# Kernel optimization log

Hardware: AMD Instinct MI355X
Metric: run time of the kernel (lower is better)

The kernel has to match this reference:

```python
import jax, jax.numpy as jnp
import numpy as np

K = 1024
H = 16
HID = 4 * K
EPS = 1e-5


def _layernorm(x, g, b):
    mu = jnp.mean(x, axis=-1, keepdims=True)
    var = jnp.var(x, axis=-1, keepdims=True)
    return (x - mu) * jax.lax.rsqrt(var + EPS) * g + b


def _attention(xq, xkv, wq, wk, wv, wo, bo, causal):
    b, t, e = xq.shape
    tc = xkv.shape[1]
    h, s = H, e // H
    scale = e ** (-0.25)  # applied to both q and k, as in the original
    q = (xq @ wq).reshape(b, t, h, s) * scale
    k = (xkv @ wk).reshape(b, tc, h, s) * scale
    v = (xkv @ wv).reshape(b, tc, h, s)
    dot = jnp.einsum('bqhs,bkhs->bhqk', q, k)  # (b,h,t,tc)
    if causal:
        mask = jnp.tril(jnp.ones((t, tc), dtype=bool))
        dot = jnp.where(mask, dot, jnp.finfo(dot.dtype).min)
    att = jax.nn.softmax(dot, axis=-1)
    out = jnp.einsum('bhqk,bkhs->bqhs', att, v).reshape(b, t, e)
    return out @ wo + bo


def setup_inputs() -> dict:
    key = jax.random.key(0)
    ks = jax.random.split(key, 16)
    sd = K ** -0.5
    inp = {
        'x': jax.random.normal(ks[0], (4, 1024, K), jnp.float32),
        'context': jax.random.normal(ks[1], (4, 1024, K), jnp.float32),
        'sa_wq': jax.random.normal(ks[2], (K, K), jnp.float32) * sd,
        'sa_wk': jax.random.normal(ks[3], (K, K), jnp.float32) * sd,
        'sa_wv': jax.random.normal(ks[4], (K, K), jnp.float32) * sd,
        'sa_wo': jax.random.normal(ks[5], (K, K), jnp.float32) * sd,
        'sa_bo': jnp.zeros((K,), jnp.float32),
        'ca_wq': jax.random.normal(ks[6], (K, K), jnp.float32) * sd,
        'ca_wk': jax.random.normal(ks[7], (K, K), jnp.float32) * sd,
        'ca_wv': jax.random.normal(ks[8], (K, K), jnp.float32) * sd,
        'ca_wo': jax.random.normal(ks[9], (K, K), jnp.float32) * sd,
        'ca_bo': jnp.zeros((K,), jnp.float32),
        'n1_g': jnp.ones((K,), jnp.float32), 'n1_b': jnp.zeros((K,), jnp.float32),
        'n2_g': jnp.ones((K,), jnp.float32), 'n2_b': jnp.zeros((K,), jnp.float32),
        'n3_g': jnp.ones((K,), jnp.float32), 'n3_b': jnp.zeros((K,), jnp.float32),
        'ff_w1': jax.random.normal(ks[10], (K, HID), jnp.float32) * sd,
        'ff_b1': jnp.zeros((HID,), jnp.float32),
        'ff_w2': jax.random.normal(ks[11], (HID, K), jnp.float32) * (HID ** -0.5),
        'ff_b2': jnp.zeros((K,), jnp.float32),
    }
    return inp


def reference(x, context, sa_wq, sa_wk, sa_wv, sa_wo, sa_bo,
              ca_wq, ca_wk, ca_wv, ca_wo, ca_bo,
              n1_g, n1_b, n2_g, n2_b, n3_g, n3_b,
              ff_w1, ff_b1, ff_w2, ff_b2):
    # Masked self-attention + residual + LN (dropout is identity in eval mode)
    sa = _attention(x, x, sa_wq, sa_wk, sa_wv, sa_wo, sa_bo, causal=True)
    x = _layernorm(x + sa, n1_g, n1_b)
    # Cross-attention + residual + LN
    ca = _attention(x, context, ca_wq, ca_wk, ca_wv, ca_wo, ca_bo, causal=False)
    x = _layernorm(x + ca, n2_g, n2_b)
    # FFN + residual + LN
    ff = jax.nn.relu(x @ ff_w1 + ff_b1) @ ff_w2 + ff_b2
    x = _layernorm(x + ff, n3_g, n3_b)
    return x
```

## Files before the change

### kernel.cpp

```cpp
#include <hip/hip_runtime.h>

typedef __bf16 bf16x8 __attribute__((ext_vector_type(8)));
typedef __bf16 bf16x4 __attribute__((ext_vector_type(4)));
typedef float floatx4 __attribute__((ext_vector_type(4)));

#define EMB 1024
#define MROWS 4096
#define HIDN 4096
#define PSTRIDE ((size_t)MROWS * EMB)

__device__ __forceinline__ void load_lds16(const __bf16* g, __bf16* l) {
    __builtin_amdgcn_global_load_lds(
        (const __attribute__((address_space(1))) void*)g,
        (__attribute__((address_space(3))) void*)l, 16, 0, 0);
}

struct TJobs { const float* s[16]; __bf16* d[16]; int sld[16]; int dld[16]; };
__global__ void transpose_cast16_kernel(TJobs a) {
    __shared__ float tile[32][33];
    int jz = blockIdx.z;
    const float* in = a.s[jz];
    __bf16* out = a.d[jz];
    int sld = a.sld[jz], dld = a.dld[jz];
    int tx = threadIdx.x, ty = threadIdx.y;
    int c0 = blockIdx.x * 32, r0 = blockIdx.y * 32;
#pragma unroll
    for (int i = 0; i < 32; i += 8)
        tile[ty + i][tx] = in[(size_t)(r0 + ty + i) * sld + c0 + tx];
    __syncthreads();
#pragma unroll
    for (int i = 0; i < 32; i += 8)
        out[(size_t)(c0 + ty + i) * dld + r0 + tx] = (__bf16)tile[tx][ty + i];
}

__global__ void transpose_v_kernel(const __bf16* __restrict__ in,
                                   __bf16* __restrict__ vt, int ld, int Tc) {
    __shared__ __bf16 tile[32][33];
    int tx = threadIdx.x, ty = threadIdx.y;
    int t0 = blockIdx.x * 32, s0 = blockIdx.y * 32;
    int bh = blockIdx.z, b = bh >> 4, h = bh & 15;
#pragma unroll
    for (int i = 0; i < 32; i += 8)
        tile[ty + i][tx] = in[(size_t)(b * Tc + t0 + ty + i) * ld + h * 64 + s0 + tx];
    __syncthreads();
#pragma unroll
    for (int i = 0; i < 32; i += 8)
        vt[((size_t)bh * 64 + s0 + ty + i) * Tc + t0 + tx] = tile[tx][ty + i];
}

__global__ void cast_bf16_kernel(const float* __restrict__ in,
                                 __bf16* __restrict__ out, int n) {
    int i = (blockIdx.x * 256 + threadIdx.x) * 4;
    if (i >= n) return;
    float4 v = *(const float4*)(in + i);
    bf16x4 o;
    o[0] = (__bf16)v.x; o[1] = (__bf16)v.y; o[2] = (__bf16)v.z; o[3] = (__bf16)v.w;
    *(bf16x4*)(out + i) = o;
}

template <int RELU, int REG>
__launch_bounds__(256, 4)
__global__ void gemm_bt(const __bf16* __restrict__ A, const __bf16* __restrict__ A2,
                        int asplit, const __bf16* __restrict__ Bt,
                        __bf16* __restrict__ cb, __bf16* __restrict__ cbalt,
                        const float* __restrict__ bias,
                        int M, int N, int Kd, float scale0, float scale1,
                        int split, int fx, int fy) {
    __shared__ alignas(16) __bf16 smem[2 * 128 * 32];
    __bf16* As = smem;
    __bf16* Bs = smem + 128 * 32;
    int tid  = threadIdx.x;
    int wv   = tid >> 6, lane = tid & 63;

    int L   = blockIdx.x + gridDim.x * (blockIdx.y + gridDim.y * blockIdx.z);
    int xcd = L & 7, j = L >> 3;
    int ff  = fx * fy;
    int zw  = xcd / ff;
    int rr  = xcd % ff;
    int nxf = gridDim.x / fx;
    int bnw = (j % nxf) * fx + (rr % fx);
    int bmw = (j / nxf) * fy + (rr / fx);
    int bn  = bnw * 128, bm = bmw * 128;

    int wm   = (wv & 1) * 64, wn = (wv >> 1) * 64;
    int l16  = lane & 15, g16 = lane >> 4;

    int kc   = Kd / gridDim.z;
    int zoff = zw * kc;

    const __bf16* Ause = (bn >= asplit) ? A2 : A;

    const __bf16* ag0 = Ause + (size_t)(bm + (tid >> 2)) * Kd + zoff + (tid & 3) * 8;
    const __bf16* ag1 = ag0 + (size_t)64 * Kd;
    const __bf16* bg0 = Bt + (size_t)(bn + (tid >> 2)) * Kd + zoff + (tid & 3) * 8;
    const __bf16* bg1 = bg0 + (size_t)64 * Kd;
    __bf16* al0 = &As[tid * 8];
    __bf16* al1 = &As[2048 + tid * 8];
    __bf16* bl0 = &Bs[tid * 8];
    __bf16* bl1 = &Bs[2048 + tid * 8];

    floatx4 acc[4][4] = {};

    if (REG) {
        bf16x8 pa0 = *(const bf16x8*)ag0;
        bf16x8 pa1 = *(const bf16x8*)ag1;
        bf16x8 pb0 = *(const bf16x8*)bg0;
        bf16x8 pb1 = *(const bf16x8*)bg1;
        for (int k0 = 0; k0 < kc; k0 += 32) {
            *(bf16x8*)al0 = pa0;
            *(bf16x8*)al1 = pa1;
            *(bf16x8*)bl0 = pb0;
            *(bf16x8*)bl1 = pb1;
            if (k0 + 32 < kc) {
                ag0 += 32; ag1 += 32; bg0 += 32; bg1 += 32;
                pa0 = *(const bf16x8*)ag0;
                pa1 = *(const bf16x8*)ag1;
                pb0 = *(const bf16x8*)bg0;
                pb1 = *(const bf16x8*)bg1;
            }
            __syncthreads();
            bf16x8 af[4], bfr[4];
#pragma unroll
            for (int i = 0; i < 4; ++i)
                af[i] = *(const bf16x8*)&As[(wm + i * 16 + l16) * 32 + g16 * 8];
#pragma unroll
            for (int jj = 0; jj < 4; ++jj)
                bfr[jj] = *(const bf16x8*)&Bs[(wn + jj * 16 + l16) * 32 + g16 * 8];
#pragma unroll
            for (int i = 0; i < 4; ++i)
#pragma unroll
                for (int jj = 0; jj < 4; ++jj)
                    acc[i][jj] = __builtin_amdgcn_mfma_f32_16x16x32_bf16(af[i], bfr[jj], acc[i][jj], 0, 0, 0);
            __syncthreads();
        }
    } else {
        for (int k0 = 0; k0 < kc; k0 += 32) {
            __syncthreads();
            load_lds16(ag0, al0); load_lds16(ag1, al1);
            load_lds16(bg0, bl0); load_lds16(bg1, bl1);
            ag0 += 32; ag1 += 32; bg0 += 32; bg1 += 32;
            __syncthreads();
            bf16x8 af[4], bfr[4];
#pragma unroll
            for (int i = 0; i < 4; ++i)
                af[i] = *(const bf16x8*)&As[(wm + i * 16 + l16) * 32 + g16 * 8];
#pragma unroll
            for (int jj = 0; jj < 4; ++jj)
                bfr[jj] = *(const bf16x8*)&Bs[(wn + jj * 16 + l16) * 32 + g16 * 8];
#pragma unroll
            for (int i = 0; i < 4; ++i)
#pragma unroll
                for (int jj = 0; jj < 4; ++jj)
                    acc[i][jj] = __builtin_amdgcn_mfma_f32_16x16x32_bf16(af[i], bfr[jj], acc[i][jj], 0, 0, 0);
        }
        __syncthreads();
    }

    __bf16* Cp = (zw == 0) ? cb : cbalt + (size_t)(zw - 1) * M * N;
    const float* bz = (zw == 0) ? bias : nullptr;

    __bf16* eb = smem + wv * 2048;
    int erow = lane >> 2;
    int ecol = (lane & 3) * 16;
#pragma unroll
    for (int i = 0; i < 4; ++i) {
#pragma unroll
        for (int jj = 0; jj < 4; ++jj) {
            int col  = bn + wn + jj * 16 + l16;
            float sc = (col < split) ? scale0 : scale1;
            float bv = bz ? bz[col] : 0.f;
#pragma unroll
            for (int r = 0; r < 4; ++r) {
                float v = acc[i][jj][r] * sc + bv;
                if (RELU) v = fmaxf(v, 0.f);
                eb[(g16 * 4 + r) * 76 + jj * 16 + l16] = (__bf16)v;
            }
        }
        bf16x8 t0 = *(const bf16x8*)&eb[erow * 76 + ecol];
        bf16x8 t1 = *(const bf16x8*)&eb[erow * 76 + ecol + 8];
        size_t gb = (size_t)(bm + wm + i * 16 + erow) * N + bn + wn + ecol;
        *(bf16x8*)&Cp[gb]     = t0;
        *(bf16x8*)&Cp[gb + 8] = t1;
    }
}


#define VM4 asm volatile("s_waitcnt vmcnt(4)" ::: "memory")
#define VM0 asm volatile("s_waitcnt vmcnt(0)" ::: "memory")

#define STG(GB, HROWS, LDST, TILE)                                             \
    do {                                                                       \
        load_lds16((GB) + (size_t)(HROWS) * Kd + (TILE) * 64, (LDST) + tid8);  \
        load_lds16((GB) + (size_t)((HROWS) + 128) * Kd + (TILE) * 64,          \
                   (LDST) + 4096 + tid8);                                      \
    } while (0)

#define PHASE(ABUF, BBUF, QM, QN, STAGE, TAIL)                                  \
    {                                                                           \
        bf16x8 a_[4][2], b_[2][2];                                              \
        _Pragma("unroll")                                                       \
        for (int i2 = 0; i2 < 4; ++i2) {                                        \
            int s_ = (QM) * 128 + wr64 + i2 * 16 + l16;                         \
            a_[i2][0] = *(const bf16x8*)&(ABUF)[s_ * 64 + pa0];                 \
            a_[i2][1] = *(const bf16x8*)&(ABUF)[s_ * 64 + pa1];                 \
        }                                                                       \
        _Pragma("unroll")                                                       \
        for (int j2 = 0; j2 < 2; ++j2) {                                        \
            int s_ = (QN) * 128 + wc32 + j2 * 16 + l16;                         \
            b_[j2][0] = *(const bf16x8*)&(BBUF)[s_ * 64 + pa0];                 \
            b_[j2][1] = *(const bf16x8*)&(BBUF)[s_ * 64 + pa1];                 \
        }                                                                       \
        STAGE;                                                                  \
        __builtin_amdgcn_s_barrier();                                           \
        asm volatile("s_waitcnt lgkmcnt(0)" ::: "memory");                      \
        __builtin_amdgcn_s_setprio(1);                                          \
        _Pragma("unroll")                                                       \
        for (int i2 = 0; i2 < 4; ++i2)                                          \
            _Pragma("unroll")                                                   \
            for (int j2 = 0; j2 < 2; ++j2) {                                    \
                acc[(QM) * 4 + i2][(QN) * 2 + j2] =                             \
                    __builtin_amdgcn_mfma_f32_16x16x32_bf16(                    \
                        a_[i2][0], b_[j2][0],                                   \
                        acc[(QM) * 4 + i2][(QN) * 2 + j2], 0, 0, 0);            \
                acc[(QM) * 4 + i2][(QN) * 2 + j2] =                             \
                    __builtin_amdgcn_mfma_f32_16x16x32_bf16(                    \
                        a_[i2][1], b_[j2][1],                                   \
                        acc[(QM) * 4 + i2][(QN) * 2 + j2], 0, 0, 0);            \
            }                                                                   \
        __builtin_amdgcn_s_setprio(0);                                          \
        TAIL;                                                                   \
        __builtin_amdgcn_s_barrier();                                           \
    }

template <int RELU>
__launch_bounds__(512, 2)
__global__ void gemm256(const __bf16* __restrict__ A, const __bf16* __restrict__ A2,
                        int asplit, const __bf16* __restrict__ Bt,
                        __bf16* __restrict__ C, const float* __restrict__ bias,
                        int N, int Kd, float scale0, float scale1,
                        int split, int pw) {
    __shared__ alignas(16) __bf16 smem[65536];
    __bf16* Alds0 = smem;
    __bf16* Alds1 = smem + 16384;
    __bf16* Blds0 = smem + 32768;
    __bf16* Blds1 = smem + 49152;

    int tid = threadIdx.x;
    int wv = tid >> 6, lane = tid & 63;
    int l16 = lane & 15, g16 = lane >> 4;
    int wr = wv >> 2, wc = wv & 3;
    int wr64 = wr * 64, wc32 = wc * 32;
    int pa0 = (g16 ^ (l16 & 7)) * 8;
    int pa1 = pa0 ^ 32;

    int L = blockIdx.x;
    int xcd = L & 7, jj = L >> 3;
    int bm = ((xcd >> 1) * 4 + jj / pw) * 256;
    int bn = ((xcd & 1) * pw + jj % pw) * 256;

    const __bf16* Ause = (bn >= asplit) ? A2 : A;
    int tid8 = tid * 8;
    int colOff = ((tid & 7) ^ ((tid >> 3) & 7)) * 8;
    const __bf16* baseA = Ause + (size_t)(bm + (tid >> 3)) * Kd + colOff;
    const __bf16* baseB = Bt + (size_t)(bn + (tid >> 8) * 64 + ((tid >> 3) & 31)) * Kd + colOff;

    floatx4 acc[8][4] = {};

    STG(baseA, 0,  Alds0,        0);
    STG(baseB, 0,  Blds0,        0);
    STG(baseA, 64, Alds0 + 8192, 0);
    STG(baseB, 32, Blds0 + 8192, 0);
    STG(baseA, 0,  Alds1,        1);
    STG(baseB, 0,  Blds1,        1);
    VM4;
    __builtin_amdgcn_s_barrier();

    int niter = Kd >> 7;
    for (int t = 0; t < niter - 1; ++t) {
        int tv = 2 * t + 1, tn0 = 2 * t + 2, tn1 = 2 * t + 3;
        PHASE(Alds0, Blds0, 0, 0, STG(baseA, 64, Alds1 + 8192, tv),  (void)0);
        PHASE(Alds0, Blds0, 0, 1, STG(baseB, 32, Blds1 + 8192, tv),  (void)0);
        PHASE(Alds0, Blds0, 1, 0, STG(baseA, 0,  Alds0,        tn0), (void)0);
        PHASE(Alds0, Blds0, 1, 1, STG(baseB, 0,  Blds0,        tn0), VM4);
        PHASE(Alds1, Blds1, 0, 0, STG(baseA, 64, Alds0 + 8192, tn0), (void)0);
        PHASE(Alds1, Blds1, 0, 1, STG(baseB, 32, Blds0 + 8192, tn0), (void)0);
        PHASE(Alds1, Blds1, 1, 0, STG(baseA, 0,  Alds1,        tn1), (void)0);
        PHASE(Alds1, Blds1, 1, 1, STG(baseB, 0,  Blds1,        tn1), VM4);
    }
    {
        int tv = (Kd >> 6) - 1;
        PHASE(Alds0, Blds0, 0, 0, STG(baseA, 64, Alds1 + 8192, tv), (void)0);
        PHASE(Alds0, Blds0, 0, 1, STG(baseB, 32, Blds1 + 8192, tv), (void)0);
        PHASE(Alds0, Blds0, 1, 0, (void)0, (void)0);
        PHASE(Alds0, Blds0, 1, 1, (void)0, VM0);
        PHASE(Alds1, Blds1, 0, 0, (void)0, (void)0);
        PHASE(Alds1, Blds1, 0, 1, (void)0, (void)0);
        PHASE(Alds1, Blds1, 1, 0, (void)0, (void)0);
        PHASE(Alds1, Blds1, 1, 1, (void)0, (void)0);
    }

    __syncthreads();

    __bf16* eb = smem + wv * 1216;
    int erow = lane >> 2;
    int ecol = (lane & 3) * 16;
    float sc[4], bv[4];
#pragma unroll
    for (int j = 0; j < 4; ++j) {
        int col = bn + wc * 64 + j * 16 + l16;
        sc[j] = (col < split) ? scale0 : scale1;
        bv[j] = bias ? bias[col] : 0.f;
    }
#pragma unroll
    for (int i = 0; i < 8; ++i) {
#pragma unroll
        for (int j = 0; j < 4; ++j) {
#pragma unroll
            for (int r = 0; r < 4; ++r) {
                float v = acc[i][j][r] * sc[j] + bv[j];
                if (RELU) v = fmaxf(v, 0.f);
                eb[(g16 * 4 + r) * 76 + j * 16 + l16] = (__bf16)v;
            }
        }
        bf16x8 t0 = *(const bf16x8*)&eb[erow * 76 + ecol];
        bf16x8 t1 = *(const bf16x8*)&eb[erow * 76 + ecol + 8];
        size_t gb = (size_t)(bm + wr * 128 + i * 16 + erow) * N + bn + wc * 64 + ecol;
        *(bf16x8*)&C[gb]     = t0;
        *(bf16x8*)&C[gb + 8] = t1;
    }
}

__launch_bounds__(256, 3)
__global__ void attn_kernel(const __bf16* __restrict__ qb, const __bf16* __restrict__ kb,
                            const __bf16* __restrict__ vt, int ldq, int ldk,
                            __bf16* __restrict__ out, int causal, int Tc) {
    constexpr int T = 1024;
    __shared__ alignas(16) __bf16 Qs[128 * 72];
    __shared__ alignas(16) __bf16 Ks[64 * 72];
    __shared__ alignas(16) __bf16 Vs[64 * 72];
    __shared__ alignas(16) __bf16 Ps[4][16 * 72];

    int tid = threadIdx.x;
    int wv = tid >> 6, lane = tid & 63;
    int l16 = lane & 15, g16 = lane >> 4;

    int L = blockIdx.x;
    int xcd = L & 7, idx = L >> 3;
    int i3 = idx & 7;
    int qt2 = (idx & 32) ? (7 - i3) : i3;
    int pair = xcd + 8 * (idx >> 3);
    int h = pair & 15, b = pair >> 4;

    int r0 = tid >> 3, s8 = (tid & 7) * 8;
    int r1 = r0 + 32;

#pragma unroll
    for (int p = 0; p < 4; ++p) {
        int row = r0 + p * 32;
        bf16x8 qv = *(const bf16x8*)(qb + (size_t)(b * T + qt2 * 128 + row) * ldq + h * 64 + s8);
        *(bf16x8*)&Qs[row * 72 + s8] = qv;
    }

    floatx4 oacc[2][4] = {};
    float li[2] = {0.f, 0.f};

    int ktend = causal ? (2 * qt2 + 2) : (Tc / 64);

    const __bf16* kbase = kb + (size_t)b * Tc * ldk + h * 64 + s8;
    const __bf16* vbase = vt + (size_t)(b * 16 + h) * 64 * Tc + s8;

    bf16x8 kc0 = *(const bf16x8*)(kbase + (size_t)r0 * ldk);
    bf16x8 kc1 = *(const bf16x8*)(kbase + (size_t)r1 * ldk);
    bf16x8 vc0 = *(const bf16x8*)(vbase + (size_t)r0 * Tc);
    bf16x8 vc1 = *(const bf16x8*)(vbase + (size_t)r1 * Tc);
    bf16x8 kn0, kn1, vn0, vn1;

    for (int kt = 0; kt < ktend; ++kt) {
        __syncthreads();
        *(bf16x8*)&Ks[r0 * 72 + s8] = kc0;
        *(bf16x8*)&Ks[r1 * 72 + s8] = kc1;
        *(bf16x8*)&Vs[r0 * 72 + s8] = vc0;
        *(bf16x8*)&Vs[r1 * 72 + s8] = vc1;
        if (kt + 1 < ktend) {
            const __bf16* kp = kbase + (size_t)(kt + 1) * 64 * ldk;
            const __bf16* vp = vbase + (size_t)(kt + 1) * 64;
            kn0 = *(const bf16x8*)(kp + (size_t)r0 * ldk);
            kn1 = *(const bf16x8*)(kp + (size_t)r1 * ldk);
            vn0 = *(const bf16x8*)(vp + (size_t)r0 * Tc);
            vn1 = *(const bf16x8*)(vp + (size_t)r1 * Tc);
        }
        __syncthreads();

#pragma unroll
        for (int sub = 0; sub < 2; ++sub) {
            if (causal && kt > 2 * qt2 + sub) continue;

            floatx4 sacc[4] = {};
#pragma unroll
            for (int kk = 0; kk < 2; ++kk) {
                bf16x8 bq = *(const bf16x8*)&Qs[(sub * 64 + wv * 16 + l16) * 72 + kk * 32 + g16 * 8];
#pragma unroll
                for (int j = 0; j < 4; ++j) {
                    bf16x8 ak = *(const bf16x8*)&Ks[(j * 16 + l16) * 72 + kk * 32 + g16 * 8];
                    sacc[j] = __builtin_amdgcn_mfma_f32_16x16x32_bf16(ak, bq, sacc[j], 0, 0, 0);
                }
            }
            if (causal && kt == 2 * qt2 + sub) {
                int qloc = wv * 16 + l16;
#pragma unroll
                for (int j = 0; j < 4; ++j)
#pragma unroll
                    for (int r = 0; r < 4; ++r)
                        if (j * 16 + g16 * 4 + r > qloc) sacc[j][r] = -1e30f;
            }

#pragma unroll
            for (int j = 0; j < 4; ++j) {
                bf16x4 pk;
#pragma unroll
                for (int r = 0; r < 4; ++r) {
                    float p = __builtin_amdgcn_exp2f(sacc[j][r]);
                    li[sub] += p;
                    pk[r] = (__bf16)p;
                }
                *(bf16x4*)&Ps[wv][l16 * 72 + j * 16 + g16 * 4] = pk;
            }
#pragma unroll
            for (int kk = 0; kk < 2; ++kk) {
                bf16x8 bp = *(const bf16x8*)&Ps[wv][l16 * 72 + kk * 32 + g16 * 8];
#pragma unroll
                for (int j = 0; j < 4; ++j) {
                    bf16x8 av = *(const bf16x8*)&Vs[(j * 16 + l16) * 72 + kk * 32 + g16 * 8];
                    oacc[sub][j] = __builtin_amdgcn_mfma_f32_16x16x32_bf16(av, bp, oacc[sub][j], 0, 0, 0);
                }
            }
        }
        kc0 = kn0; kc1 = kn1; vc0 = vn0; vc1 = vn1;
    }

    li[0] += __shfl_xor(li[0], 16); li[0] += __shfl_xor(li[0], 32);
    li[1] += __shfl_xor(li[1], 16); li[1] += __shfl_xor(li[1], 32);

    __syncthreads();
    int rw = lane >> 2, c4 = (lane & 3) * 16;
#pragma unroll
    for (int sub = 0; sub < 2; ++sub) {
        float inv = 1.f / li[sub];
#pragma unroll
        for (int j = 0; j < 4; ++j) {
            bf16x4 ok;
#pragma unroll
            for (int r = 0; r < 4; ++r) ok[r] = (__bf16)(oacc[sub][j][r] * inv);
            *(bf16x4*)&Ks[(wv * 16 + l16) * 72 + j * 16 + g16 * 4] = ok;
        }
        bf16x8 o0 = *(const bf16x8*)&Ks[(wv * 16 + rw) * 72 + c4];
        bf16x8 o1 = *(const bf16x8*)&Ks[(wv * 16 + rw) * 72 + c4 + 8];
        size_t ob = (size_t)(b * T + qt2 * 128 + sub * 64 + wv * 16 + rw) * EMB + h * 64 + c4;
        *(bf16x8*)&out[ob]     = o0;
        *(bf16x8*)&out[ob + 8] = o1;
    }
}

__launch_bounds__(256)
__global__ void ln_kernel(const float* __restrict__ res,
                          const __bf16* __restrict__ pb, int np,
                          const float* __restrict__ g, const float* __restrict__ be,
                          float* __restrict__ outf, __bf16* __restrict__ outb) {
    __shared__ float red[8];
    int row = blockIdx.x, tid = threadIdx.x;
    size_t base = (size_t)row * EMB;
    float4 v = ((const float4*)(res + base))[tid];
    for (int i = 0; i < np; ++i) {
        bf16x4 u = *(const bf16x4*)(pb + i * PSTRIDE + base + tid * 4);
        v.x += (float)u[0]; v.y += (float)u[1];
        v.z += (float)u[2]; v.w += (float)u[3];
    }
    float s  = v.x + v.y + v.z + v.w;
    float ss = v.x * v.x + v.y * v.y + v.z * v.z + v.w * v.w;
#pragma unroll
    for (int o = 1; o < 64; o <<= 1) { s += __shfl_xor(s, o); ss += __shfl_xor(ss, o); }
    if ((tid & 63) == 0) { red[(tid >> 6) * 2] = s; red[(tid >> 6) * 2 + 1] = ss; }
    __syncthreads();
    s  = red[0] + red[2] + red[4] + red[6];
    ss = red[1] + red[3] + red[5] + red[7];
    float mu  = s * (1.0f / 1024.0f);
    float var = ss * (1.0f / 1024.0f) - mu * mu;
    float rs  = rsqrtf(var + 1e-5f);
    float4 gg = ((const float4*)g)[tid];
    float4 bb = ((const float4*)be)[tid];
    float4 y;
    y.x = (v.x - mu) * rs * gg.x + bb.x;
    y.y = (v.y - mu) * rs * gg.y + bb.y;
    y.z = (v.z - mu) * rs * gg.z + bb.z;
    y.w = (v.w - mu) * rs * gg.w + bb.w;
    ((float4*)(outf + base))[tid] = y;
    if (outb) {
        bf16x4 o;
        o[0] = (__bf16)y.x; o[1] = (__bf16)y.y; o[2] = (__bf16)y.z; o[3] = (__bf16)y.w;
        *(bf16x4*)(outb + base + tid * 4) = o;
    }
}

extern "C" void kernel_launch(void* const* d_in, const int* in_sizes, int n_in,
                              void* d_out, int out_size, void* d_ws, size_t ws_size,
                              hipStream_t stream) {
    const float* x     = (const float*)d_in[0];
    const float* ctx   = (const float*)d_in[1];
    const float* sa_wq = (const float*)d_in[2];
    const float* sa_wk = (const float*)d_in[3];
    const float* sa_wv = (const float*)d_in[4];
    const float* sa_wo = (const float*)d_in[5];
    const float* sa_bo = (const float*)d_in[6];
    const float* ca_wq = (const float*)d_in[7];
    const float* ca_wk = (const float*)d_in[8];
    const float* ca_wv = (const float*)d_in[9];
    const float* ca_wo = (const float*)d_in[10];
    const float* ca_bo = (const float*)d_in[11];
    const float* n1_g = (const float*)d_in[12];
    const float* n1_b = (const float*)d_in[13];
    const float* n2_g = (const float*)d_in[14];
    const float* n2_b = (const float*)d_in[15];
    const float* n3_g = (const float*)d_in[16];
    const float* n3_b = (const float*)d_in[17];
    const float* ff_w1 = (const float*)d_in[18];
    const float* ff_b1 = (const float*)d_in[19];
    const float* ff_w2 = (const float*)d_in[20];
    const float* ff_b2 = (const float*)d_in[21];

    size_t off = 0;
    auto alloc = [&](size_t bytes) {
        void* p = (char*)d_ws + off;
        off += (bytes + 255) & ~(size_t)255;
        return p;
    };
    __bf16* w_sa_qkvT = (__bf16*)alloc((size_t)3 * EMB * EMB * 2);
    __bf16* w_sa_oT   = (__bf16*)alloc((size_t)EMB * EMB * 2);
    __bf16* w_ca_kvqT = (__bf16*)alloc((size_t)3 * EMB * EMB * 2);
    __bf16* w_ca_oT   = (__bf16*)alloc((size_t)EMB * EMB * 2);
    __bf16* w1T       = (__bf16*)alloc((size_t)HIDN * EMB * 2);
    __bf16* w2T       = (__bf16*)alloc((size_t)EMB * HIDN * 2);
    __bf16* xb        = (__bf16*)alloc((size_t)MROWS * EMB * 2);
    __bf16* qkv       = (__bf16*)alloc((size_t)MROWS * 3 * EMB * 2);
    __bf16* ao        = (__bf16*)alloc((size_t)MROWS * EMB * 2);
    __bf16* hid       = (__bf16*)alloc((size_t)MROWS * HIDN * 2);
    __bf16* x1b       = (__bf16*)alloc((size_t)MROWS * EMB * 2);
    __bf16* vt        = (__bf16*)alloc((size_t)MROWS * EMB * 2);
    float* res1       = (float*)alloc((size_t)MROWS * EMB * 4);
    float* res2       = (float*)alloc((size_t)MROWS * EMB * 4);

    __bf16* qkvc = qkv;
    __bf16* pbo  = qkv;
    __bf16* pbf  = xb;

    const float QSC = 0.04508422002778011f;
    const int   BIG = 1 << 30;
    dim3 tb(32, 8);

    TJobs tj;
    tj.s[0] = sa_wq; tj.d[0] = w_sa_qkvT;                          tj.sld[0] = EMB;  tj.dld[0] = EMB;
    tj.s[1] = sa_wk; tj.d[1] = w_sa_qkvT + (size_t)EMB * EMB;      tj.sld[1] = EMB;  tj.dld[1] = EMB;
    tj.s[2] = sa_wv; tj.d[2] = w_sa_qkvT + (size_t)2 * EMB * EMB;  tj.sld[2] = EMB;  tj.dld[2] = EMB;
    tj.s[3] = sa_wo; tj.d[3] = w_sa_oT;                            tj.sld[3] = EMB;  tj.dld[3] = EMB;
    tj.s[4] = ca_wk; tj.d[4] = w_ca_kvqT;                          tj.sld[4] = EMB;  tj.dld[4] = EMB;
    tj.s[5] = ca_wv; tj.d[5] = w_ca_kvqT + (size_t)EMB * EMB;      tj.sld[5] = EMB;  tj.dld[5] = EMB;
    tj.s[6] = ca_wq; tj.d[6] = w_ca_kvqT + (size_t)2 * EMB * EMB;  tj.sld[6] = EMB;  tj.dld[6] = EMB;
    tj.s[7] = ca_wo; tj.d[7] = w_ca_oT;                            tj.sld[7] = EMB;  tj.dld[7] = EMB;
    for (int c = 0; c < 4; ++c) {
        tj.s[8 + c] = ff_w1 + (size_t)c * 1024;
        tj.d[8 + c] = w1T + (size_t)c * 1024 * 1024;
        tj.sld[8 + c] = HIDN; tj.dld[8 + c] = EMB;
    }
    for (int c = 0; c < 4; ++c) {
        tj.s[12 + c] = ff_w2 + (size_t)c * 1024 * 1024;
        tj.d[12 + c] = w2T + (size_t)c * 1024;
        tj.sld[12 + c] = EMB; tj.dld[12 + c] = HIDN;
    }
    transpose_cast16_kernel<<<dim3(32, 32, 16), tb, 0, stream>>>(tj);

    cast_bf16_kernel<<<4096, 256, 0, stream>>>(x, xb, MROWS * EMB);
    gemm256<0><<<192, 512, 0, stream>>>(xb, xb, BIG, w_sa_qkvT,
        qkv, nullptr, 3 * EMB, EMB, QSC, 1.f, 1024, 6);
    transpose_v_kernel<<<dim3(32, 2, 64), tb, 0, stream>>>(qkv + 2 * EMB, vt, 3 * EMB, 1024);
    attn_kernel<<<512, 256, 0, stream>>>(qkv, qkv + EMB, vt, 3 * EMB, 3 * EMB, ao, 1, 1024);
    gemm_bt<0, 1><<<dim3(8, 32, 2), 256, 0, stream>>>(ao, ao, BIG, w_sa_oT,
        pbo, pbo + PSTRIDE, sa_bo, MROWS, EMB, EMB, 1.f, 1.f, 0, 2, 2);
    ln_kernel<<<4096, 256, 0, stream>>>(x, pbo, 2, n1_g, n1_b, res1, x1b);

    cast_bf16_kernel<<<4096, 256, 0, stream>>>(ctx, xb, MROWS * EMB);
    gemm256<0><<<192, 512, 0, stream>>>(xb, x1b, 2048, w_ca_kvqT,
        qkvc, nullptr, 3 * EMB, EMB, 1.f, QSC, 2048, 6);
    transpose_v_kernel<<<dim3(32, 2, 64), tb, 0, stream>>>(qkvc + EMB, vt, 3 * EMB, 1024);
    attn_kernel<<<512, 256, 0, stream>>>(qkvc + 2 * EMB, qkvc, vt, 3 * EMB, 3 * EMB, ao, 0, 1024);
    gemm_bt<0, 1><<<dim3(8, 32, 2), 256, 0, stream>>>(ao, ao, BIG, w_ca_oT,
        pbo, pbo + PSTRIDE, ca_bo, MROWS, EMB, EMB, 1.f, 1.f, 0, 2, 2);
    ln_kernel<<<4096, 256, 0, stream>>>(res1, pbo, 2, n2_g, n2_b, res2, x1b);

    gemm256<1><<<256, 512, 0, stream>>>(x1b, x1b, BIG, w1T,
        hid, ff_b1, HIDN, EMB, 1.f, 1.f, 0, 8);
    gemm_bt<0, 1><<<dim3(8, 32, 4), 256, 0, stream>>>(hid, hid, BIG, w2T,
        pbf, pbf + PSTRIDE, ff_b2, MROWS, EMB, HIDN, 1.f, 1.f, 0, 1, 2);
    ln_kernel<<<4096, 256, 0, stream>>>(res2, pbf, 4, n3_g, n3_b, (float*)d_out, nullptr);
}
```

Before: 461.7 us.

## Use split-K gemm256 for FFN down-projection and reuse B fragments across phases

Adds split-K support to the 256x256 gemm256 kernel through blockIdx.y, with each K-slice writing a bf16 partial to its own buffer and only the first slice adding bias. The FFN second matmul now uses this kernel with four K-splits instead of gemm_bt, so its partials are still summed in the layernorm. The inner loop also keeps two sets of B-fragment registers, so each B sub-tile is read from LDS once and reused across both M halves instead of being reloaded. The extra live registers could push against the launch bound of two blocks per CU. The 64x4 grid gives 256 workgroups on the larger tile.

```diff
diff --git a/kernel.cpp b/kernel.cpp
--- a/kernel.cpp
+++ b/kernel.cpp
@@ -195,21 +195,24 @@
                    (LDST) + 4096 + tid8);                                      \
     } while (0)
 
-#define PHASE(ABUF, BBUF, QM, QN, STAGE, TAIL)                                  \
+#define RD_A(ABUF, QM)                                                         \
+    _Pragma("unroll")                                                          \
+    for (int i2 = 0; i2 < 4; ++i2) {                                           \
+        int s_ = (QM) * 128 + wr64 + i2 * 16 + l16;                            \
+        a_[i2][0] = *(const bf16x8*)&(ABUF)[s_ * 64 + pa0];                    \
+        a_[i2][1] = *(const bf16x8*)&(ABUF)[s_ * 64 + pa1];                    \
+    }
+
+#define RD_B(BBUF, QN, BREG)                                                   \
+    _Pragma("unroll")                                                          \
+    for (int j2 = 0; j2 < 2; ++j2) {                                           \
+        int s_ = (QN) * 128 + wc32 + j2 * 16 + l16;                            \
+        BREG[j2][0] = *(const bf16x8*)&(BBUF)[s_ * 64 + pa0];                  \
+        BREG[j2][1] = *(const bf16x8*)&(BBUF)[s_ * 64 + pa1];                  \
+    }
+
+#define CORE(QM, QN, BREG, STAGE, TAIL)                                         \
     {                                                                           \
-        bf16x8 a_[4][2], b_[2][2];                                              \
-        _Pragma("unroll")                                                       \
-        for (int i2 = 0; i2 < 4; ++i2) {                                        \
-            int s_ = (QM) * 128 + wr64 + i2 * 16 + l16;                         \
-            a_[i2][0] = *(const bf16x8*)&(ABUF)[s_ * 64 + pa0];                 \
-            a_[i2][1] = *(const bf16x8*)&(ABUF)[s_ * 64 + pa1];                 \
-        }                                                                       \
-        _Pragma("unroll")                                                       \
-        for (int j2 = 0; j2 < 2; ++j2) {                                        \
-            int s_ = (QN) * 128 + wc32 + j2 * 16 + l16;                         \
-            b_[j2][0] = *(const bf16x8*)&(BBUF)[s_ * 64 + pa0];                 \
-            b_[j2][1] = *(const bf16x8*)&(BBUF)[s_ * 64 + pa1];                 \
-        }                                                                       \
         STAGE;                                                                  \
         __builtin_amdgcn_s_barrier();                                           \
         asm volatile("s_waitcnt lgkmcnt(0)" ::: "memory");                      \
@@ -220,11 +223,11 @@
             for (int j2 = 0; j2 < 2; ++j2) {                                    \
                 acc[(QM) * 4 + i2][(QN) * 2 + j2] =                             \
                     __builtin_amdgcn_mfma_f32_16x16x32_bf16(                    \
-                        a_[i2][0], b_[j2][0],                                   \
+                        a_[i2][0], BREG[j2][0],                                 \
                         acc[(QM) * 4 + i2][(QN) * 2 + j2], 0, 0, 0);            \
                 acc[(QM) * 4 + i2][(QN) * 2 + j2] =                             \
                     __builtin_amdgcn_mfma_f32_16x16x32_bf16(                    \
-                        a_[i2][1], b_[j2][1],                                   \
+                        a_[i2][1], BREG[j2][1],                                 \
                         acc[(QM) * 4 + i2][(QN) * 2 + j2], 0, 0, 0);            \
             }                                                                   \
         __builtin_amdgcn_s_setprio(0);                                          \
@@ -236,8 +239,9 @@
 __launch_bounds__(512, 2)
 __global__ void gemm256(const __bf16* __restrict__ A, const __bf16* __restrict__ A2,
                         int asplit, const __bf16* __restrict__ Bt,
-                        __bf16* __restrict__ C, const float* __restrict__ bias,
-                        int N, int Kd, float scale0, float scale1,
+                        __bf16* __restrict__ C, __bf16* __restrict__ Calt,
+                        const float* __restrict__ bias,
+                        int M, int N, int Kd, float scale0, float scale1,
                         int split, int pw) {
     __shared__ alignas(16) __bf16 smem[65536];
     __bf16* Alds0 = smem;
@@ -258,13 +262,18 @@
     int bm = ((xcd >> 1) * 4 + jj / pw) * 256;
     int bn = ((xcd & 1) * pw + jj % pw) * 256;
 
+    int z = blockIdx.y;
+    int kc = Kd / gridDim.y;
+    int zoff = z * kc;
+
     const __bf16* Ause = (bn >= asplit) ? A2 : A;
     int tid8 = tid * 8;
     int colOff = ((tid & 7) ^ ((tid >> 3) & 7)) * 8;
-    const __bf16* baseA = Ause + (size_t)(bm + (tid >> 3)) * Kd + colOff;
-    const __bf16* baseB = Bt + (size_t)(bn + (tid >> 8) * 64 + ((tid >> 3) & 31)) * Kd + colOff;
+    const __bf16* baseA = Ause + (size_t)(bm + (tid >> 3)) * Kd + zoff + colOff;
+    const __bf16* baseB = Bt + (size_t)(bn + (tid >> 8) * 64 + ((tid >> 3) & 31)) * Kd + zoff + colOff;
 
     floatx4 acc[8][4] = {};
+    bf16x8 a_[4][2], b0_[2][2], b1_[2][2];
 
     STG(baseA, 0,  Alds0,        0);
     STG(baseB, 0,  Blds0,        0);
@@ -275,31 +284,46 @@
     VM4;
     __builtin_amdgcn_s_barrier();
 
-    int niter = Kd >> 7;
+    int niter = kc >> 7;
     for (int t = 0; t < niter - 1; ++t) {
         int tv = 2 * t + 1, tn0 = 2 * t + 2, tn1 = 2 * t + 3;
-        PHASE(Alds0, Blds0, 0, 0, STG(baseA, 64, Alds1 + 8192, tv),  (void)0);
-        PHASE(Alds0, Blds0, 0, 1, STG(baseB, 32, Blds1 + 8192, tv),  (void)0);
-        PHASE(Alds0, Blds0, 1, 0, STG(baseA, 0,  Alds0,        tn0), (void)0);
-        PHASE(Alds0, Blds0, 1, 1, STG(baseB, 0,  Blds0,        tn0), VM4);
-        PHASE(Alds1, Blds1, 0, 0, STG(baseA, 64, Alds0 + 8192, tn0), (void)0);
-        PHASE(Alds1, Blds1, 0, 1, STG(baseB, 32, Blds0 + 8192, tn0), (void)0);
-        PHASE(Alds1, Blds1, 1, 0, STG(baseA, 0,  Alds1,        tn1), (void)0);
-        PHASE(Alds1, Blds1, 1, 1, STG(baseB, 0,  Blds1,        tn1), VM4);
+        RD_A(Alds0, 0); RD_B(Blds0, 0, b0_);
+        CORE(0, 0, b0_, STG(baseA, 64, Alds1 + 8192, tv),  (void)0);
+        RD_B(Blds0, 1, b1_);
+        CORE(0, 1, b1_, STG(baseB, 32, Blds1 + 8192, tv),  (void)0);
+        RD_A(Alds0, 1);
+        CORE(1, 0, b0_, STG(baseA, 0,  Alds0,        tn0), (void)0);
+        CORE(1, 1, b1_, STG(baseB, 0,  Blds0,        tn0), VM4);
+        RD_A(Alds1, 0); RD_B(Blds1, 0, b0_);
+        CORE(0, 0, b0_, STG(baseA, 64, Alds0 + 8192, tn0), (void)0);
+        RD_B(Blds1, 1, b1_);
+        CORE(0, 1, b1_, STG(baseB, 32, Blds0 + 8192, tn0), (void)0);
+        RD_A(Alds1, 1);
+        CORE(1, 0, b0_, STG(baseA, 0,  Alds1,        tn1), (void)0);
+        CORE(1, 1, b1_, STG(baseB, 0,  Blds1,        tn1), VM4);
     }
     {
-        int tv = (Kd >> 6) - 1;
-        PHASE(Alds0, Blds0, 0, 0, STG(baseA, 64, Alds1 + 8192, tv), (void)0);
-        PHASE(Alds0, Blds0, 0, 1, STG(baseB, 32, Blds1 + 8192, tv), (void)0);
-        PHASE(Alds0, Blds0, 1, 0, (void)0, (void)0);
-        PHASE(Alds0, Blds0, 1, 1, (void)0, VM0);
-        PHASE(Alds1, Blds1, 0, 0, (void)0, (void)0);
-        PHASE(Alds1, Blds1, 0, 1, (void)0, (void)0);
-        PHASE(Alds1, Blds1, 1, 0, (void)0, (void)0);
-        PHASE(Alds1, Blds1, 1, 1, (void)0, (void)0);
+        int tv = (kc >> 6) - 1;
+        RD_A(Alds0, 0); RD_B(Blds0, 0, b0_);
+        CORE(0, 0, b0_, STG(baseA, 64, Alds1 + 8192, tv), (void)0);
+        RD_B(Blds0, 1, b1_);
+        CORE(0, 1, b1_, STG(baseB, 32, Blds1 + 8192, tv), (void)0);
+        RD_A(Alds0, 1);
+        CORE(1, 0, b0_, (void)0, (void)0);
+        CORE(1, 1, b1_, (void)0, VM0);
+        RD_A(Alds1, 0); RD_B(Blds1, 0, b0_);
+        CORE(0, 0, b0_, (void)0, (void)0);
+        RD_B(Blds1, 1, b1_);
+        CORE(0, 1, b1_, (void)0, (void)0);
+        RD_A(Alds1, 1);
+        CORE(1, 0, b0_, (void)0, (void)0);
+        CORE(1, 1, b1_, (void)0, (void)0);
     }
 
     __syncthreads();
+
+    __bf16* Cp = (z == 0) ? C : Calt + (size_t)(z - 1) * M * N;
+    const float* bz = (z == 0) ? bias : nullptr;
 
     __bf16* eb = smem + wv * 1216;
     int erow = lane >> 2;
@@ -309,7 +333,7 @@
     for (int j = 0; j < 4; ++j) {
         int col = bn + wc * 64 + j * 16 + l16;
         sc[j] = (col < split) ? scale0 : scale1;
-        bv[j] = bias ? bias[col] : 0.f;
+        bv[j] = bz ? bz[col] : 0.f;
     }
 #pragma unroll
     for (int i = 0; i < 8; ++i) {
@@ -325,8 +349,8 @@
         bf16x8 t0 = *(const bf16x8*)&eb[erow * 76 + ecol];
         bf16x8 t1 = *(const bf16x8*)&eb[erow * 76 + ecol + 8];
         size_t gb = (size_t)(bm + wr * 128 + i * 16 + erow) * N + bn + wc * 64 + ecol;
-        *(bf16x8*)&C[gb]     = t0;
-        *(bf16x8*)&C[gb + 8] = t1;
+        *(bf16x8*)&Cp[gb]     = t0;
+        *(bf16x8*)&Cp[gb + 8] = t1;
     }
 }
 
@@ -579,7 +603,7 @@
 
     cast_bf16_kernel<<<4096, 256, 0, stream>>>(x, xb, MROWS * EMB);
     gemm256<0><<<192, 512, 0, stream>>>(xb, xb, BIG, w_sa_qkvT,
-        qkv, nullptr, 3 * EMB, EMB, QSC, 1.f, 1024, 6);
+        qkv, nullptr, nullptr, MROWS, 3 * EMB, EMB, QSC, 1.f, 1024, 6);
     transpose_v_kernel<<<dim3(32, 2, 64), tb, 0, stream>>>(qkv + 2 * EMB, vt, 3 * EMB, 1024);
     attn_kernel<<<512, 256, 0, stream>>>(qkv, qkv + EMB, vt, 3 * EMB, 3 * EMB, ao, 1, 1024);
     gemm_bt<0, 1><<<dim3(8, 32, 2), 256, 0, stream>>>(ao, ao, BIG, w_sa_oT,
@@ -588,7 +612,7 @@
 
     cast_bf16_kernel<<<4096, 256, 0, stream>>>(ctx, xb, MROWS * EMB);
     gemm256<0><<<192, 512, 0, stream>>>(xb, x1b, 2048, w_ca_kvqT,
-        qkvc, nullptr, 3 * EMB, EMB, 1.f, QSC, 2048, 6);
+        qkvc, nullptr, nullptr, MROWS, 3 * EMB, EMB, 1.f, QSC, 2048, 6);
     transpose_v_kernel<<<dim3(32, 2, 64), tb, 0, stream>>>(qkvc + EMB, vt, 3 * EMB, 1024);
     attn_kernel<<<512, 256, 0, stream>>>(qkvc + 2 * EMB, qkvc, vt, 3 * EMB, 3 * EMB, ao, 0, 1024);
     gemm_bt<0, 1><<<dim3(8, 32, 2), 256, 0, stream>>>(ao, ao, BIG, w_ca_oT,
@@ -596,8 +620,8 @@
     ln_kernel<<<4096, 256, 0, stream>>>(res1, pbo, 2, n2_g, n2_b, res2, x1b);
 
     gemm256<1><<<256, 512, 0, stream>>>(x1b, x1b, BIG, w1T,
-        hid, ff_b1, HIDN, EMB, 1.f, 1.f, 0, 8);
-    gemm_bt<0, 1><<<dim3(8, 32, 4), 256, 0, stream>>>(hid, hid, BIG, w2T,
-        pbf, pbf + PSTRIDE, ff_b2, MROWS, EMB, HIDN, 1.f, 1.f, 0, 1, 2);
+        hid, nullptr, ff_b1, MROWS, HIDN, EMB, 1.f, 1.f, 0, 8);
+    gemm256<0><<<dim3(64, 4), 512, 0, stream>>>(hid, hid, BIG, w2T,
+        pbf, pbf + PSTRIDE, ff_b2, MROWS, EMB, HIDN, 1.f, 1.f, 0, 2);
     ln_kernel<<<4096, 256, 0, stream>>>(res2, pbf, 4, n3_g, n3_b, (float*)d_out, nullptr);
 }
```

Measured after the change: 443.4 us. -4.0%, faster.
